# Kernel tuning notes

Hardware: AMD Instinct MI355X
Metric: run time of the kernel (lower is better)

The kernel has to match this reference:

```python
import jax, jax.numpy as jnp
import numpy as np

B, S, H, I, E, K = 4, 2048, 2048, 5632, 8, 2


def setup_inputs() -> dict:
    key = jax.random.key(0)
    k0, k1, k2, k3, k4 = jax.random.split(key, 5)
    std_p = 1.0 / np.sqrt(H)
    return {
        "hidden_states": jax.random.normal(k0, (B, S, H), dtype=jnp.float32),
        "router_w": jax.random.normal(k1, (E, H), dtype=jnp.float32) * 0.02,
        "w_gate": jax.random.normal(k2, (E, H, I), dtype=jnp.float32) * std_p,
        "w_up": jax.random.normal(k3, (E, H, I), dtype=jnp.float32) * std_p,
        "w_down": jax.random.normal(k4, (E, I, H), dtype=jnp.float32) * (1.0 / np.sqrt(I)),
    }


def reference(hidden_states, router_w, w_gate, w_up, w_down):
    b, s, h = hidden_states.shape
    x = hidden_states.reshape(-1, h)                       # [T, H]
    router_logits = x @ router_w.T                          # [T, E]
    routing_weights = jax.nn.softmax(router_logits, axis=-1)
    top_w, top_i = jax.lax.top_k(routing_weights, K)        # [T, K]
    top_w = top_w / jnp.sum(top_w, axis=-1, keepdims=True)  # renormalize over top-k
    # combine[t, e] = sum_k top_w[t, k] * (top_i[t, k] == e)
    combine = jnp.sum(jax.nn.one_hot(top_i, E, dtype=top_w.dtype) * top_w[..., None], axis=1)  # [T, E]
    out = jnp.zeros_like(x)
    for e in range(E):  # small fixed expert count
        # SwiGLU expert MLP: down(silu(gate(x)) * up(x))
        act = jax.nn.silu(x @ w_gate[e]) * (x @ w_up[e])    # [T, I]
        out = out + (act @ w_down[e]) * combine[:, e:e + 1]
    return (out.reshape(b, s, h),
            router_logits.reshape(b, s, E),
            top_i.reshape(b, s, K),
            top_w.reshape(b, s, K))
```

## Files before the change

kernel.cpp:

```cpp
#include <hip/hip_runtime.h>
#include <hip/hip_bf16.h>
#include <stdint.h>

#define NTOK 8192
#define HD   2048
#define ID   5632
#define NE   8
#define NASSIGN (NTOK * 2)
#define MAXT256 (NASSIGN / 256 + NE)

typedef __attribute__((ext_vector_type(8))) short  bf16x8;
typedef __attribute__((ext_vector_type(4))) float  f32x4;
typedef __attribute__((ext_vector_type(8))) unsigned short u16x8;

__device__ __forceinline__ unsigned short f2bf(float f) {
  union { float f; unsigned int u; } c; c.f = f;
  unsigned int lsb = (c.u >> 16) & 1u;
  return (unsigned short)((c.u + 0x7fffu + lsb) >> 16);
}

__device__ __forceinline__ void async16(const void* g, void* l) {
  __builtin_amdgcn_global_load_lds(
      (const __attribute__((address_space(1))) void*)g,
      (__attribute__((address_space(3))) void*)l, 16, 0, 0);
}

__global__ __launch_bounds__(256) void k_router(
    const float* __restrict__ x, const float* __restrict__ rw,
    float* __restrict__ out_logits, float* __restrict__ out_topi,
    float* __restrict__ out_topw,
    int* __restrict__ tk_e, float* __restrict__ tk_w, int* __restrict__ cnts)
{
  const int wid = threadIdx.x >> 6, lane = threadIdx.x & 63;
  const int t = blockIdx.x * 4 + wid;
  const float* xr = x + (size_t)t * HD;
  float acc[NE];
#pragma unroll
  for (int e = 0; e < NE; e++) acc[e] = 0.f;
#pragma unroll
  for (int i = 0; i < 8; i++) {
    const int col = lane * 4 + i * 256;
    const float4 xv = *(const float4*)(xr + col);
#pragma unroll
    for (int e = 0; e < NE; e++) {
      const float4 wv = *(const float4*)(rw + e * HD + col);
      acc[e] += xv.x * wv.x + xv.y * wv.y + xv.z * wv.z + xv.w * wv.w;
    }
  }
#pragma unroll
  for (int e = 0; e < NE; e++)
    for (int o = 32; o >= 1; o >>= 1) acc[e] += __shfl_xor(acc[e], o, 64);

  if (lane == 0) {
    int i1 = 0;
#pragma unroll
    for (int e = 1; e < NE; e++) if (acc[e] > acc[i1]) i1 = e;
    int i2 = (i1 == 0) ? 1 : 0;
#pragma unroll
    for (int e = 0; e < NE; e++) if (e != i1 && acc[e] > acc[i2]) i2 = e;
    float p2 = __expf(acc[i2] - acc[i1]);
    float s  = 1.f + p2;
    float w1 = 1.f / s, w2 = p2 / s;
#pragma unroll
    for (int e = 0; e < NE; e++) out_logits[(size_t)t * NE + e] = acc[e];
    out_topi[t * 2 + 0] = (float)i1; out_topi[t * 2 + 1] = (float)i2;
    out_topw[t * 2 + 0] = w1;        out_topw[t * 2 + 1] = w2;
    tk_e[t * 2 + 0] = i1; tk_e[t * 2 + 1] = i2;
    tk_w[t * 2 + 0] = w1; tk_w[t * 2 + 1] = w2;
    atomicAdd(&cnts[i1], 1); atomicAdd(&cnts[i2], 1);
  }
}

__global__ void k_scan(const int* __restrict__ cnts, int* __restrict__ offs,
                       int* __restrict__ cursor, int* __restrict__ tile_e,
                       int* __restrict__ tile_rt, int* __restrict__ ntiles) {
  if (threadIdx.x == 0) {
    int s = 0, nt = 0;
    for (int e = 0; e < NE; e++) {
      offs[e] = s; cursor[e] = s;
      int ntl = (cnts[e] + 255) >> 8;
      for (int i = 0; i < ntl; i++) { tile_e[nt] = e; tile_rt[nt] = i; nt++; }
      s += cnts[e];
    }
    ntiles[0] = nt;
  }
}

__global__ void k_assign(const int* __restrict__ tk_e, const float* __restrict__ tk_w,
                         int* __restrict__ cursor, int* __restrict__ perm,
                         float* __restrict__ pw, int* __restrict__ inv) {
  int t = blockIdx.x * 256 + threadIdx.x;
  if (t >= NTOK) return;
#pragma unroll
  for (int k = 0; k < 2; k++) {
    int e = tk_e[t * 2 + k];
    int pos = atomicAdd(&cursor[e], 1);
    perm[pos] = t;
    pw[pos] = tk_w[t * 2 + k];
    inv[t * 2 + k] = pos;
  }
}

__global__ __launch_bounds__(256) void k_gather(const float* __restrict__ x,
    const int* __restrict__ perm, unsigned short* __restrict__ xg) {
  const int r = blockIdx.x;
  const int tok = perm[r];
  const float* src = x + (size_t)tok * HD;
  unsigned short* dst = xg + (size_t)r * HD;
  const int c = threadIdx.x * 8;
  float4 a = *(const float4*)(src + c);
  float4 b = *(const float4*)(src + c + 4);
  u16x8 o;
  o[0] = f2bf(a.x); o[1] = f2bf(a.y); o[2] = f2bf(a.z); o[3] = f2bf(a.w);
  o[4] = f2bf(b.x); o[5] = f2bf(b.y); o[6] = f2bf(b.z); o[7] = f2bf(b.w);
  *(u16x8*)(dst + c) = o;
}

__global__ __launch_bounds__(256) void k_conv64(const float* __restrict__ in0,
    const float* __restrict__ in1, unsigned short* __restrict__ out0,
    unsigned short* __restrict__ out1, int R, int C, int nmat) {
  __shared__ unsigned short tlb[64][72];
  const int z = blockIdx.z;
  const int mat = (nmat == 2) ? (z & 1) : 0;
  const int e   = (nmat == 2) ? (z >> 1) : z;
  const float* in = ((mat == 0) ? in0 : in1) + (size_t)e * R * C;
  unsigned short* out = ((mat == 0) ? out0 : out1) + (size_t)e * (size_t)R * C;
  const int tid = threadIdx.x;
  const int c0 = blockIdx.x * 64, r0 = blockIdx.y * 64;
#pragma unroll
  for (int pass = 0; pass < 4; ++pass) {
    const int kr = pass * 16 + (tid >> 4);
    const int cc = (tid & 15) * 4;
    const float4 v = *(const float4*)(in + (size_t)(r0 + kr) * C + c0 + cc);
    tlb[cc + 0][kr] = f2bf(v.x); tlb[cc + 1][kr] = f2bf(v.y);
    tlb[cc + 2][kr] = f2bf(v.z); tlb[cc + 3][kr] = f2bf(v.w);
  }
  __syncthreads();
#pragma unroll
  for (int pass = 0; pass < 2; ++pass) {
    const int n = pass * 32 + (tid >> 3);
    const int k = (tid & 7) * 8;
    *(u16x8*)(out + (size_t)(c0 + n) * R + r0 + k) = *(const u16x8*)&tlb[n][k];
  }
}

#define HBF(b,kh) (((b)*2+(kh))*32768)

__global__ __launch_bounds__(512, 2) void k_gemm_gu256f(
    const unsigned short* __restrict__ A,
    const unsigned short* __restrict__ BgT, const unsigned short* __restrict__ BuT,
    const int* __restrict__ cnts, const int* __restrict__ offs,
    const int* __restrict__ tile_e, const int* __restrict__ tile_rt,
    const int* __restrict__ ntiles, unsigned short* __restrict__ gact)
{
  const int raw = blockIdx.x;
  const int v = (raw & 7) * ((int)gridDim.x >> 3) + (raw >> 3);
  const int ct = v / MAXT256;
  const int ti = v % MAXT256;
  if (ti >= ntiles[0]) return;
  const int e = tile_e[ti], rt = tile_rt[ti];
  const int cnt = cnts[e], off = offs[e];
  const int tid = threadIdx.x;

  __shared__ __align__(16) char smem[131072];

  const unsigned short* Bg = BgT + (size_t)e * (size_t)ID * HD;
  const unsigned short* Bu = BuT + (size_t)e * (size_t)ID * HD;
  const size_t arow0 = (size_t)off + (size_t)rt * 256;
  const size_t bcol0 = (size_t)ct * 128;

  const int r0s = tid >> 2;
  const int c0s = (((tid & 3) ^ ((tid >> 3) & 3)) * 8);

  const int NT = HD / 64, NIT = NT / 2;

  auto STAGE_A = [&](int bb, int kh, int kt) {
    const int kc = kt * 64 + kh * 32;
    async16(A + (arow0 + r0s) * (size_t)HD + kc + c0s, smem + HBF(bb,kh) + tid * 16);
    async16(A + (arow0 + 128 + r0s) * (size_t)HD + kc + c0s, smem + HBF(bb,kh) + 8192 + tid * 16);
  };
  auto STAGE_B = [&](int bb, int kh, int kt) {
    const int kc = kt * 64 + kh * 32;
    async16(Bg + (bcol0 + r0s) * (size_t)HD + kc + c0s, smem + HBF(bb,kh) + 16384 + tid * 16);
    async16(Bu + (bcol0 + r0s) * (size_t)HD + kc + c0s, smem + HBF(bb,kh) + 24576 + tid * 16);
  };

  f32x4 accg[8][2], accu[8][2];
#pragma unroll
  for (int m = 0; m < 8; m++)
#pragma unroll
    for (int n = 0; n < 2; n++) { accg[m][n] = (f32x4)0.f; accu[m][n] = (f32x4)0.f; }

  const int lane = tid & 63, wid = tid >> 6;
  const int wm = wid >> 2, wn = wid & 3;
  const int fr = lane & 15;
  const int slot = ((lane >> 4) ^ ((fr >> 1) & 3));
  const int laddr = (fr << 6) + (slot << 4);

  STAGE_A(0,0,0); STAGE_B(0,0,0); STAGE_A(0,1,0); STAGE_B(0,1,0);
  STAGE_A(1,0,1); STAGE_B(1,0,1);
  asm volatile("s_waitcnt vmcnt(4)" ::: "memory");
  asm volatile("s_barrier" ::: "memory");

  constexpr int SB[8]  = {1,1,0,0,0,0,1,1};
  constexpr int SOP[8] = {0,1,0,1,0,1,0,1};
  constexpr int SKH[8] = {1,1,0,0,1,1,0,0};
  constexpr int SKO[8] = {1,1,2,2,2,2,3,3};

  bf16x8 bgr[2], bur[2];
  for (int i = 0; i < NIT; ++i) {
#pragma unroll
    for (int p = 0; p < 8; ++p) {
      const int b = p >> 2, kh = (p >> 1) & 1, mh = p & 1;
      bf16x8 afr[4];
#pragma unroll
      for (int t = 0; t < 4; t++)
        afr[t] = *(const bf16x8*)(smem + HBF(b,kh) + ((wm*128 + mh*64 + t*16) << 6) + laddr);
      if (mh == 0) {
#pragma unroll
        for (int t = 0; t < 2; t++) {
          bgr[t] = *(const bf16x8*)(smem + HBF(b,kh) + 16384 + ((wn*32 + t*16) << 6) + laddr);
          bur[t] = *(const bf16x8*)(smem + HBF(b,kh) + 24576 + ((wn*32 + t*16) << 6) + laddr);
        }
      }
      {
        int kt = 2 * i + SKO[p]; kt = kt < NT - 1 ? kt : NT - 1;
        if (SOP[p] == 0) STAGE_A(SB[p], SKH[p], kt);
        else             STAGE_B(SB[p], SKH[p], kt);
      }
      asm volatile("s_barrier" ::: "memory");
      __builtin_amdgcn_s_setprio(1);
#pragma unroll
      for (int t = 0; t < 4; t++)
#pragma unroll
        for (int n = 0; n < 2; n++) {
          accg[mh*4 + t][n] = __builtin_amdgcn_mfma_f32_16x16x32_bf16(afr[t], bgr[n], accg[mh*4 + t][n], 0, 0, 0);
          accu[mh*4 + t][n] = __builtin_amdgcn_mfma_f32_16x16x32_bf16(afr[t], bur[n], accu[mh*4 + t][n], 0, 0, 0);
        }
      __builtin_amdgcn_s_setprio(0);
      if (p == 3 || p == 7) asm volatile("s_waitcnt vmcnt(4)" ::: "memory");
      asm volatile("s_barrier" ::: "memory");
    }
  }
  asm volatile("s_waitcnt vmcnt(0)" ::: "memory");

  const int crow = (lane >> 4) * 4, ccol = lane & 15;
  const int rbase = rt * 256 + wm * 128;
#pragma unroll
  for (int mt = 0; mt < 8; ++mt) {
#pragma unroll
    for (int j = 0; j < 4; ++j) {
      const int rl = rbase + mt * 16 + crow + j;
      if (rl >= cnt) continue;
      const size_t grow = (size_t)off + rl;
#pragma unroll
      for (int nt = 0; nt < 2; ++nt) {
        const int col = (int)bcol0 + wn * 32 + nt * 16 + ccol;
        const float g = accg[mt][nt][j], u = accu[mt][nt][j];
        const float a = g / (1.f + __expf(-g)) * u;
        gact[grow * (size_t)ID + col] = f2bf(a);
      }
    }
  }
}

#define HB(b,kh,op) (((((b)*2+(kh))*2)+(op))*16384)

__global__ __launch_bounds__(512, 2) void k_gemm_dn256(
    const unsigned short* __restrict__ A,
    const unsigned short* __restrict__ Wbase,
    const int* __restrict__ cnts, const int* __restrict__ offs,
    const int* __restrict__ tile_e, const int* __restrict__ tile_rt,
    const int* __restrict__ ntiles,
    const float* __restrict__ pw, float* __restrict__ dbuf)
{
  const int raw = blockIdx.x;
  const int v = (raw & 7) * ((int)gridDim.x >> 3) + (raw >> 3);
  const int ct = v / MAXT256;
  const int ti = v % MAXT256;
  if (ti >= ntiles[0]) return;
  const int e = tile_e[ti], rt = tile_rt[ti];
  const int cnt = cnts[e], off = offs[e];
  const int tid = threadIdx.x;

  __shared__ __align__(16) char smem[131072];

  const unsigned short* W = Wbase + (size_t)e * (size_t)HD * ID;
  const size_t arow0 = (size_t)off + (size_t)rt * 256;
  const size_t bcol0 = (size_t)ct * 256;

  const int r0s = tid >> 2;
  const int c0s = (((tid & 3) ^ ((tid >> 3) & 3)) * 8);

  const int NT = ID / 64, NIT = NT / 2;

  auto STAGE_A = [&](int bb, int kh, int kt) {
    const int kc = kt * 64 + kh * 32;
    async16(A + (arow0 + r0s) * (size_t)ID + kc + c0s, smem + HB(bb,kh,0) + tid * 16);
    async16(A + (arow0 + 128 + r0s) * (size_t)ID + kc + c0s, smem + HB(bb,kh,0) + 8192 + tid * 16);
  };
  auto STAGE_B = [&](int bb, int kh, int kt) {
    const int kc = kt * 64 + kh * 32;
    async16(W + (bcol0 + r0s) * (size_t)ID + kc + c0s, smem + HB(bb,kh,1) + tid * 16);
    async16(W + (bcol0 + 128 + r0s) * (size_t)ID + kc + c0s, smem + HB(bb,kh,1) + 8192 + tid * 16);
  };

  f32x4 acc[8][4];
#pragma unroll
  for (int m = 0; m < 8; m++)
#pragma unroll
    for (int n = 0; n < 4; n++) acc[m][n] = (f32x4)0.f;

  const int lane = tid & 63, wid = tid >> 6;
  const int wm = wid >> 2, wn = wid & 3;
  const int fr = lane & 15;
  const int slot = ((lane >> 4) ^ ((fr >> 1) & 3));
  const int laddr = (fr << 6) + (slot << 4);

  STAGE_A(0,0,0); STAGE_B(0,0,0); STAGE_A(0,1,0); STAGE_B(0,1,0);
  STAGE_A(1,0,1); STAGE_B(1,0,1);
  asm volatile("s_waitcnt vmcnt(4)" ::: "memory");
  asm volatile("s_barrier" ::: "memory");

  constexpr int SB[8]  = {1,1,0,0,0,0,1,1};
  constexpr int SOP[8] = {0,1,0,1,0,1,0,1};
  constexpr int SKH[8] = {1,1,0,0,1,1,0,0};
  constexpr int SKO[8] = {1,1,2,2,2,2,3,3};

  bf16x8 bfr[4];
  for (int i = 0; i < NIT; ++i) {
#pragma unroll
    for (int p = 0; p < 8; ++p) {
      const int b = p >> 2, kh = (p >> 1) & 1, mh = p & 1;
      bf16x8 afr[4];
#pragma unroll
      for (int t = 0; t < 4; t++)
        afr[t] = *(const bf16x8*)(smem + HB(b,kh,0) + ((wm*128 + mh*64 + t*16) << 6) + laddr);
      if (mh == 0) {
#pragma unroll
        for (int t = 0; t < 4; t++)
          bfr[t] = *(const bf16x8*)(smem + HB(b,kh,1) + ((wn*64 + t*16) << 6) + laddr);
      }
      {
        int kt = 2 * i + SKO[p]; kt = kt < NT - 1 ? kt : NT - 1;
        if (SOP[p] == 0) STAGE_A(SB[p], SKH[p], kt);
        else             STAGE_B(SB[p], SKH[p], kt);
      }
      asm volatile("s_barrier" ::: "memory");
      __builtin_amdgcn_s_setprio(1);
#pragma unroll
      for (int t = 0; t < 4; t++)
#pragma unroll
        for (int n = 0; n < 4; n++)
          acc[mh*4 + t][n] = __builtin_amdgcn_mfma_f32_16x16x32_bf16(afr[t], bfr[n], acc[mh*4 + t][n], 0, 0, 0);
      __builtin_amdgcn_s_setprio(0);
      if (p == 3 || p == 7) asm volatile("s_waitcnt vmcnt(4)" ::: "memory");
      asm volatile("s_barrier" ::: "memory");
    }
  }
  asm volatile("s_waitcnt vmcnt(0)" ::: "memory");

  const int crow = (lane >> 4) * 4, ccol = lane & 15;
  const int rbase = rt * 256 + wm * 128;
#pragma unroll
  for (int mt = 0; mt < 8; ++mt) {
#pragma unroll
    for (int j = 0; j < 4; ++j) {
      const int rl = rbase + mt * 16 + crow + j;
      if (rl >= cnt) continue;
      const size_t grow = (size_t)off + rl;
      const float wgt = pw[grow];
#pragma unroll
      for (int nt = 0; nt < 4; ++nt) {
        const int col = (int)bcol0 + wn * 64 + nt * 16 + ccol;
        dbuf[grow * (size_t)HD + col] = acc[mt][nt][j] * wgt;
      }
    }
  }
}

__global__ __launch_bounds__(256) void k_combine(const float* __restrict__ dbuf,
    const int* __restrict__ inv, float* __restrict__ out) {
  const int t = blockIdx.x;
  const int p0 = inv[t * 2], p1 = inv[t * 2 + 1];
  const float4* r0 = (const float4*)(dbuf + (size_t)p0 * HD);
  const float4* r1 = (const float4*)(dbuf + (size_t)p1 * HD);
  float4* o = (float4*)(out + (size_t)t * HD);
#pragma unroll
  for (int i = 0; i < 2; i++) {
    int c = threadIdx.x + i * 256;
    float4 a = r0[c], b = r1[c];
    o[c] = make_float4(a.x + b.x, a.y + b.y, a.z + b.z, a.w + b.w);
  }
}

extern "C" void kernel_launch(void* const* d_in, const int* in_sizes, int n_in,
                              void* d_out, int out_size, void* d_ws, size_t ws_size,
                              hipStream_t stream) {
  const float* x  = (const float*)d_in[0];
  const float* rw = (const float*)d_in[1];
  const float* wg = (const float*)d_in[2];
  const float* wu = (const float*)d_in[3];
  const float* wd = (const float*)d_in[4];

  float* outp       = (float*)d_out;
  float* out_logits = outp + (size_t)NTOK * HD;
  float* out_topi   = out_logits + (size_t)NTOK * NE;
  float* out_topw   = out_topi + (size_t)NTOK * 2;

  char* w = (char*)d_ws;
  int*   cnts    = (int*)(w + 0);
  int*   offs    = (int*)(w + 64);
  int*   cursor  = (int*)(w + 128);
  int*   ntiles  = (int*)(w + 192);
  int*   tile_e  = (int*)(w + 256);
  int*   tile_rt = (int*)(w + 1280);
  int*   tk_e    = (int*)(w + 4096);
  float* tk_w    = (float*)(w + 4096 + 65536);
  int*   perm    = (int*)(w + 4096 + 2 * 65536);
  float* pw      = (float*)(w + 4096 + 3 * 65536);
  int*   inv     = (int*)(w + 4096 + 4 * 65536);

  char* big = w + (1 << 20);
  unsigned short* xg = (unsigned short*)big;
  const size_t XG_E = (size_t)(NASSIGN + 256) * HD;
  unsigned short* wgT = xg + XG_E;
  const size_t WT_E = (size_t)NE * ID * HD;
  unsigned short* wuT  = wgT + WT_E;
  unsigned short* wdT  = wuT + WT_E;
  unsigned short* gact = wdT + WT_E;
  const size_t GA_E = (size_t)(NASSIGN + 256) * ID;
  float* dbuf = (float*)(gact + GA_E);

  hipMemsetAsync(d_ws, 0, 256, stream);

  k_conv64<<<dim3(ID / 64, HD / 64, 2 * NE), 256, 0, stream>>>(
      wg, wu, wgT, wuT, HD, ID, 2);
  k_conv64<<<dim3(HD / 64, ID / 64, NE), 256, 0, stream>>>(
      wd, nullptr, wdT, nullptr, ID, HD, 1);

  k_router<<<NTOK / 4, 256, 0, stream>>>(x, rw, out_logits, out_topi, out_topw,
                                         tk_e, tk_w, cnts);
  k_scan<<<1, 64, 0, stream>>>(cnts, offs, cursor, tile_e, tile_rt, ntiles);
  k_assign<<<NTOK / 256, 256, 0, stream>>>(tk_e, tk_w, cursor, perm, pw, inv);
  k_gather<<<NASSIGN, 256, 0, stream>>>(x, perm, xg);

  k_gemm_gu256f<<<dim3((ID / 128) * MAXT256), 512, 0, stream>>>(
      xg, wgT, wuT, cnts, offs, tile_e, tile_rt, ntiles, gact);
  k_gemm_dn256<<<dim3((HD / 256) * MAXT256), 512, 0, stream>>>(
      gact, wdT, cnts, offs, tile_e, tile_rt, ntiles, pw, dbuf);
  k_combine<<<NTOK, 256, 0, stream>>>(dbuf, inv, outp);
}
```

Before: 1.855 ms.

## Switch expert GEMMs to 32x32x16 MFMA and split-K the down projection

Both expert GEMMs now use the 32x32x16 bf16 MFMA with matching swizzled LDS fragment loads and epilogue row mapping, replacing the 16x16x32 tiles. The intent is fewer LDS fragment reads per unit of MFMA work. The down-projection GEMM is also split along K into two halves, doubling its grid, and each half writes its own fp32 partial buffer. The combine kernel then sums four partial rows per token. This buys better CU fill for the down GEMM at the cost of an extra full fp32 partial buffer write and read, and it assumes the workspace can hold the second buffer.

```diff
diff --git a/kernel.cpp b/kernel.cpp
--- a/kernel.cpp
+++ b/kernel.cpp
@@ -9,9 +9,10 @@
 #define NASSIGN (NTOK * 2)
 #define MAXT256 (NASSIGN / 256 + NE)
 
-typedef __attribute__((ext_vector_type(8))) short  bf16x8;
-typedef __attribute__((ext_vector_type(4))) float  f32x4;
-typedef __attribute__((ext_vector_type(8))) unsigned short u16x8;
+typedef __attribute__((ext_vector_type(8)))  short bf16x8;
+typedef __attribute__((ext_vector_type(4)))  float f32x4;
+typedef __attribute__((ext_vector_type(16))) float f32x16;
+typedef __attribute__((ext_vector_type(8)))  unsigned short u16x8;
 
 __device__ __forceinline__ unsigned short f2bf(float f) {
   union { float f; unsigned int u; } c; c.f = f;
@@ -185,17 +186,14 @@
     async16(Bu + (bcol0 + r0s) * (size_t)HD + kc + c0s, smem + HBF(bb,kh) + 24576 + tid * 16);
   };
 
-  f32x4 accg[8][2], accu[8][2];
-#pragma unroll
-  for (int m = 0; m < 8; m++)
-#pragma unroll
-    for (int n = 0; n < 2; n++) { accg[m][n] = (f32x4)0.f; accu[m][n] = (f32x4)0.f; }
+  f32x16 accg[4], accu[4];
+#pragma unroll
+  for (int m = 0; m < 4; m++) { accg[m] = (f32x16)0.f; accu[m] = (f32x16)0.f; }
 
   const int lane = tid & 63, wid = tid >> 6;
   const int wm = wid >> 2, wn = wid & 3;
-  const int fr = lane & 15;
-  const int slot = ((lane >> 4) ^ ((fr >> 1) & 3));
-  const int laddr = (fr << 6) + (slot << 4);
+  const int lrow = lane & 31, lx = lane >> 5;
+  const int lswz = (lrow >> 1) & 3;
 
   STAGE_A(0,0,0); STAGE_B(0,0,0); STAGE_A(0,1,0); STAGE_B(0,1,0);
   STAGE_A(1,0,1); STAGE_B(1,0,1);
@@ -212,15 +210,21 @@
 #pragma unroll
     for (int p = 0; p < 8; ++p) {
       const int b = p >> 2, kh = (p >> 1) & 1, mh = p & 1;
-      bf16x8 afr[4];
-#pragma unroll
-      for (int t = 0; t < 4; t++)
-        afr[t] = *(const bf16x8*)(smem + HBF(b,kh) + ((wm*128 + mh*64 + t*16) << 6) + laddr);
+      bf16x8 afr[2][2];
+#pragma unroll
+      for (int mt2 = 0; mt2 < 2; mt2++)
+#pragma unroll
+        for (int ks = 0; ks < 2; ks++)
+          afr[mt2][ks] = *(const bf16x8*)(smem + HBF(b,kh)
+              + ((wm*128 + mh*64 + mt2*32 + lrow) << 6)
+              + ((((ks << 1) + lx) ^ lswz) << 4));
       if (mh == 0) {
 #pragma unroll
-        for (int t = 0; t < 2; t++) {
-          bgr[t] = *(const bf16x8*)(smem + HBF(b,kh) + 16384 + ((wn*32 + t*16) << 6) + laddr);
-          bur[t] = *(const bf16x8*)(smem + HBF(b,kh) + 24576 + ((wn*32 + t*16) << 6) + laddr);
+        for (int ks = 0; ks < 2; ks++) {
+          bgr[ks] = *(const bf16x8*)(smem + HBF(b,kh) + 16384
+              + ((wn*32 + lrow) << 6) + ((((ks << 1) + lx) ^ lswz) << 4));
+          bur[ks] = *(const bf16x8*)(smem + HBF(b,kh) + 24576
+              + ((wn*32 + lrow) << 6) + ((((ks << 1) + lx) ^ lswz) << 4));
         }
       }
       {
@@ -231,11 +235,13 @@
       asm volatile("s_barrier" ::: "memory");
       __builtin_amdgcn_s_setprio(1);
 #pragma unroll
-      for (int t = 0; t < 4; t++)
-#pragma unroll
-        for (int n = 0; n < 2; n++) {
-          accg[mh*4 + t][n] = __builtin_amdgcn_mfma_f32_16x16x32_bf16(afr[t], bgr[n], accg[mh*4 + t][n], 0, 0, 0);
-          accu[mh*4 + t][n] = __builtin_amdgcn_mfma_f32_16x16x32_bf16(afr[t], bur[n], accu[mh*4 + t][n], 0, 0, 0);
+      for (int mt2 = 0; mt2 < 2; mt2++)
+#pragma unroll
+        for (int ks = 0; ks < 2; ks++) {
+          accg[mh*2 + mt2] = __builtin_amdgcn_mfma_f32_32x32x16_bf16(
+              afr[mt2][ks], bgr[ks], accg[mh*2 + mt2], 0, 0, 0);
+          accu[mh*2 + mt2] = __builtin_amdgcn_mfma_f32_32x32x16_bf16(
+              afr[mt2][ks], bur[ks], accu[mh*2 + mt2], 0, 0, 0);
         }
       __builtin_amdgcn_s_setprio(0);
       if (p == 3 || p == 7) asm volatile("s_waitcnt vmcnt(4)" ::: "memory");
@@ -244,22 +250,19 @@
   }
   asm volatile("s_waitcnt vmcnt(0)" ::: "memory");
 
-  const int crow = (lane >> 4) * 4, ccol = lane & 15;
+  const int ccol = lane & 31, rsub = (lane >> 5) * 4;
   const int rbase = rt * 256 + wm * 128;
-#pragma unroll
-  for (int mt = 0; mt < 8; ++mt) {
-#pragma unroll
-    for (int j = 0; j < 4; ++j) {
-      const int rl = rbase + mt * 16 + crow + j;
+  const int col = (int)bcol0 + wn * 32 + ccol;
+#pragma unroll
+  for (int mt = 0; mt < 4; ++mt) {
+#pragma unroll
+    for (int j = 0; j < 16; ++j) {
+      const int rl = rbase + mt * 32 + (j & 3) + ((j >> 2) << 3) + rsub;
       if (rl >= cnt) continue;
       const size_t grow = (size_t)off + rl;
-#pragma unroll
-      for (int nt = 0; nt < 2; ++nt) {
-        const int col = (int)bcol0 + wn * 32 + nt * 16 + ccol;
-        const float g = accg[mt][nt][j], u = accu[mt][nt][j];
-        const float a = g / (1.f + __expf(-g)) * u;
-        gact[grow * (size_t)ID + col] = f2bf(a);
-      }
+      const float g = accg[mt][j], u = accu[mt][j];
+      const float a = g / (1.f + __expf(-g)) * u;
+      gact[grow * (size_t)ID + col] = f2bf(a);
     }
   }
 }
@@ -276,8 +279,10 @@
 {
   const int raw = blockIdx.x;
   const int v = (raw & 7) * ((int)gridDim.x >> 3) + (raw >> 3);
-  const int ct = v / MAXT256;
   const int ti = v % MAXT256;
+  const int rest = v / MAXT256;
+  const int ksplit = rest & 1;
+  const int ct = rest >> 1;
   if (ti >= ntiles[0]) return;
   const int e = tile_e[ti], rt = tile_rt[ti];
   const int cnt = cnts[e], off = offs[e];
@@ -288,34 +293,34 @@
   const unsigned short* W = Wbase + (size_t)e * (size_t)HD * ID;
   const size_t arow0 = (size_t)off + (size_t)rt * 256;
   const size_t bcol0 = (size_t)ct * 256;
+  const int kbase = ksplit * (ID / 2);
 
   const int r0s = tid >> 2;
   const int c0s = (((tid & 3) ^ ((tid >> 3) & 3)) * 8);
 
-  const int NT = ID / 64, NIT = NT / 2;
+  const int NT = (ID / 2) / 64, NIT = NT / 2;
 
   auto STAGE_A = [&](int bb, int kh, int kt) {
-    const int kc = kt * 64 + kh * 32;
+    const int kc = kbase + kt * 64 + kh * 32;
     async16(A + (arow0 + r0s) * (size_t)ID + kc + c0s, smem + HB(bb,kh,0) + tid * 16);
     async16(A + (arow0 + 128 + r0s) * (size_t)ID + kc + c0s, smem + HB(bb,kh,0) + 8192 + tid * 16);
   };
   auto STAGE_B = [&](int bb, int kh, int kt) {
-    const int kc = kt * 64 + kh * 32;
+    const int kc = kbase + kt * 64 + kh * 32;
     async16(W + (bcol0 + r0s) * (size_t)ID + kc + c0s, smem + HB(bb,kh,1) + tid * 16);
     async16(W + (bcol0 + 128 + r0s) * (size_t)ID + kc + c0s, smem + HB(bb,kh,1) + 8192 + tid * 16);
   };
 
-  f32x4 acc[8][4];
-#pragma unroll
-  for (int m = 0; m < 8; m++)
-#pragma unroll
-    for (int n = 0; n < 4; n++) acc[m][n] = (f32x4)0.f;
+  f32x16 acc[4][2];
+#pragma unroll
+  for (int m = 0; m < 4; m++)
+#pragma unroll
+    for (int n = 0; n < 2; n++) acc[m][n] = (f32x16)0.f;
 
   const int lane = tid & 63, wid = tid >> 6;
   const int wm = wid >> 2, wn = wid & 3;
-  const int fr = lane & 15;
-  const int slot = ((lane >> 4) ^ ((fr >> 1) & 3));
-  const int laddr = (fr << 6) + (slot << 4);
+  const int lrow = lane & 31, lx = lane >> 5;
+  const int lswz = (lrow >> 1) & 3;
 
   STAGE_A(0,0,0); STAGE_B(0,0,0); STAGE_A(0,1,0); STAGE_B(0,1,0);
   STAGE_A(1,0,1); STAGE_B(1,0,1);
@@ -327,19 +332,27 @@
   constexpr int SKH[8] = {1,1,0,0,1,1,0,0};
   constexpr int SKO[8] = {1,1,2,2,2,2,3,3};
 
-  bf16x8 bfr[4];
+  bf16x8 bfr[2][2];
   for (int i = 0; i < NIT; ++i) {
 #pragma unroll
     for (int p = 0; p < 8; ++p) {
       const int b = p >> 2, kh = (p >> 1) & 1, mh = p & 1;
-      bf16x8 afr[4];
-#pragma unroll
-      for (int t = 0; t < 4; t++)
-        afr[t] = *(const bf16x8*)(smem + HB(b,kh,0) + ((wm*128 + mh*64 + t*16) << 6) + laddr);
+      bf16x8 afr[2][2];
+#pragma unroll
+      for (int mt2 = 0; mt2 < 2; mt2++)
+#pragma unroll
+        for (int ks = 0; ks < 2; ks++)
+          afr[mt2][ks] = *(const bf16x8*)(smem + HB(b,kh,0)
+              + ((wm*128 + mh*64 + mt2*32 + lrow) << 6)
+              + ((((ks << 1) + lx) ^ lswz) << 4));
       if (mh == 0) {
 #pragma unroll
-        for (int t = 0; t < 4; t++)
-          bfr[t] = *(const bf16x8*)(smem + HB(b,kh,1) + ((wn*64 + t*16) << 6) + laddr);
+        for (int nt = 0; nt < 2; nt++)
+#pragma unroll
+          for (int ks = 0; ks < 2; ks++)
+            bfr[nt][ks] = *(const bf16x8*)(smem + HB(b,kh,1)
+                + ((wn*64 + nt*32 + lrow) << 6)
+                + ((((ks << 1) + lx) ^ lswz) << 4));
       }
       {
         int kt = 2 * i + SKO[p]; kt = kt < NT - 1 ? kt : NT - 1;
@@ -349,10 +362,13 @@
       asm volatile("s_barrier" ::: "memory");
       __builtin_amdgcn_s_setprio(1);
 #pragma unroll
-      for (int t = 0; t < 4; t++)
-#pragma unroll
-        for (int n = 0; n < 4; n++)
-          acc[mh*4 + t][n] = __builtin_amdgcn_mfma_f32_16x16x32_bf16(afr[t], bfr[n], acc[mh*4 + t][n], 0, 0, 0);
+      for (int mt2 = 0; mt2 < 2; mt2++)
+#pragma unroll
+        for (int nt = 0; nt < 2; nt++)
+#pragma unroll
+          for (int ks = 0; ks < 2; ks++)
+            acc[mh*2 + mt2][nt] = __builtin_amdgcn_mfma_f32_32x32x16_bf16(
+                afr[mt2][ks], bfr[nt][ks], acc[mh*2 + mt2][nt], 0, 0, 0);
       __builtin_amdgcn_s_setprio(0);
       if (p == 3 || p == 7) asm volatile("s_waitcnt vmcnt(4)" ::: "memory");
       asm volatile("s_barrier" ::: "memory");
@@ -360,20 +376,21 @@
   }
   asm volatile("s_waitcnt vmcnt(0)" ::: "memory");
 
-  const int crow = (lane >> 4) * 4, ccol = lane & 15;
+  float* db = dbuf + (size_t)ksplit * (size_t)NASSIGN * HD;
+  const int ccol = lane & 31, rsub = (lane >> 5) * 4;
   const int rbase = rt * 256 + wm * 128;
 #pragma unroll
-  for (int mt = 0; mt < 8; ++mt) {
-#pragma unroll
-    for (int j = 0; j < 4; ++j) {
-      const int rl = rbase + mt * 16 + crow + j;
+  for (int mt = 0; mt < 4; ++mt) {
+#pragma unroll
+    for (int j = 0; j < 16; ++j) {
+      const int rl = rbase + mt * 32 + (j & 3) + ((j >> 2) << 3) + rsub;
       if (rl >= cnt) continue;
       const size_t grow = (size_t)off + rl;
       const float wgt = pw[grow];
 #pragma unroll
-      for (int nt = 0; nt < 4; ++nt) {
-        const int col = (int)bcol0 + wn * 64 + nt * 16 + ccol;
-        dbuf[grow * (size_t)HD + col] = acc[mt][nt][j] * wgt;
+      for (int nt = 0; nt < 2; ++nt) {
+        const int col = (int)bcol0 + wn * 64 + nt * 32 + ccol;
+        db[grow * (size_t)HD + col] = acc[mt][nt][j] * wgt;
       }
     }
   }
@@ -383,14 +400,18 @@
     const int* __restrict__ inv, float* __restrict__ out) {
   const int t = blockIdx.x;
   const int p0 = inv[t * 2], p1 = inv[t * 2 + 1];
-  const float4* r0 = (const float4*)(dbuf + (size_t)p0 * HD);
-  const float4* r1 = (const float4*)(dbuf + (size_t)p1 * HD);
+  const float* d1 = dbuf + (size_t)NASSIGN * HD;
+  const float4* a0 = (const float4*)(dbuf + (size_t)p0 * HD);
+  const float4* a1 = (const float4*)(dbuf + (size_t)p1 * HD);
+  const float4* b0 = (const float4*)(d1 + (size_t)p0 * HD);
+  const float4* b1 = (const float4*)(d1 + (size_t)p1 * HD);
   float4* o = (float4*)(out + (size_t)t * HD);
 #pragma unroll
   for (int i = 0; i < 2; i++) {
     int c = threadIdx.x + i * 256;
-    float4 a = r0[c], b = r1[c];
-    o[c] = make_float4(a.x + b.x, a.y + b.y, a.z + b.z, a.w + b.w);
+    float4 x0 = a0[c], x1 = a1[c], y0 = b0[c], y1 = b1[c];
+    o[c] = make_float4(x0.x + x1.x + y0.x + y1.x, x0.y + x1.y + y0.y + y1.y,
+                       x0.z + x1.z + y0.z + y1.z, x0.w + x1.w + y0.w + y1.w);
   }
 }
 
@@ -447,7 +468,7 @@
 
   k_gemm_gu256f<<<dim3((ID / 128) * MAXT256), 512, 0, stream>>>(
       xg, wgT, wuT, cnts, offs, tile_e, tile_rt, ntiles, gact);
-  k_gemm_dn256<<<dim3((HD / 256) * MAXT256), 512, 0, stream>>>(
+  k_gemm_dn256<<<dim3((HD / 256) * 2 * MAXT256), 512, 0, stream>>>(
       gact, wdT, cnts, offs, tile_e, tile_rt, ntiles, pw, dbuf);
   k_combine<<<NTOK, 256, 0, stream>>>(dbuf, inv, outp);
 }
```

After: 1.995 ms. 7.6% more time.
